# Performance work log

Hardware: AMD Instinct MI355X
Metric: run time of the kernel (lower is better)

Reference implementation:

```python
import jax, jax.numpy as jnp
import numpy as np

# --- static config (matches init_kwargs) ---
CHUNK = 128
MAX_K_QK, MAX_K_V, MAX_K_KNOW = 32, 32, 64
CAND_MULT = 2
N_HEADS = 16


def threshold_gate(scores, tau, max_k):
    """scores:[B,C,N], tau:[B,C,1] -> sparse normalized gates."""
    raw = scores - tau
    gate = jnp.where(raw > 0, raw, 1e-8 * jnp.exp(raw))
    eg = jnp.exp(gate) - 1.0
    topk_vals, _ = jax.lax.top_k(eg, max_k)
    eg = jnp.where(eg >= topk_vals[..., -1:], eg, 0.0)
    gate_sum = eg.sum(axis=-1, keepdims=True) + 1e-8
    gate_strength = jnp.tanh(eg.max(axis=-1, keepdims=True))
    return eg / gate_sum * gate_strength


def _chunked(a, n_chunks):
    B, S = a.shape[0], a.shape[1]
    return a.reshape(B, n_chunks, CHUNK, -1).transpose(1, 0, 2, 3)  # [nc,B,C,*]


def _unchunk(a):
    nc, B, C, D = a.shape
    return a.transpose(1, 0, 2, 3).reshape(B, nc * C, D)


def attn_pipeline(x, qk_pos, v_pos, tau_q, tau_k, tau_v, qk_neurons, v_neurons,
                  npos_qk, npos_v, expand_O):
    B, S, D = x.shape
    n_chunks = S // CHUNK
    n_cq = MAX_K_QK * CAND_MULT
    n_cv = MAX_K_V * CAND_MULT

    xs = (_chunked(x, n_chunks), _chunked(qk_pos, n_chunks), _chunked(v_pos, n_chunks),
          _chunked(tau_q, n_chunks), _chunked(tau_k, n_chunks), _chunked(tau_v, n_chunks))

    def chunk_fn(loss, inp):
        x_c, qp_c, vp_c, tq_c, tk_c, tv_c = inp
        # position-based candidate selection (indices are non-differentiable)
        d_qk = jnp.sum((qp_c[:, :, None, :] - npos_qk[None, None]) ** 2, axis=-1)  # [B,C,Nqk]
        _, idx_qk = jax.lax.top_k(-d_qk, n_cq)
        idx_qk = jax.lax.stop_gradient(idx_qk)
        cand_qk = qk_neurons[idx_qk]                                   # [B,C,n_cq,D]
        d_v = jnp.sum((vp_c[:, :, None, :] - npos_v[None, None]) ** 2, axis=-1)
        _, idx_v = jax.lax.top_k(-d_v, n_cv)
        idx_v = jax.lax.stop_gradient(idx_v)
        cand_v = v_neurons[idx_v]
        # scores == activations here (router dropout is identity, rate 0)
        act_qk = jnp.einsum('bsd,bsnd->bsn', x_c, cand_qk)
        act_v = jnp.einsum('bsd,bsnd->bsn', x_c, cand_v)
        gQ = threshold_gate(act_qk, tq_c, MAX_K_QK)
        gK = threshold_gate(act_qk, tk_c, MAX_K_QK)
        gV = threshold_gate(act_v, tv_c, MAX_K_V)
        Qc = jnp.einsum('bsn,bsnd->bsd', act_qk * gQ, cand_qk)
        Kc = jnp.einsum('bsn,bsnd->bsd', act_qk * gK, cand_qk)
        Vc = jnp.einsum('bsn,bsnd->bsd', act_v * gV, cand_v)
        pl_qk = (jax.lax.stop_gradient(gQ)
                 * jnp.sum((qp_c[:, :, None, :] - npos_qk[idx_qk]) ** 2, axis=-1)).mean()
        pl_v = (jax.lax.stop_gradient(gV)
                * jnp.sum((vp_c[:, :, None, :] - npos_v[idx_v]) ** 2, axis=-1)).mean()
        return loss + pl_qk + pl_v, (Qc, Kc, Vc)

    loss, (Qs, Ks, Vs) = jax.lax.scan(chunk_fn, jnp.float32(0.0), xs)
    Q, K, V = _unchunk(Qs), _unchunk(Ks), _unchunk(Vs)
    pos_loss = loss / n_chunks

    d_head = D // N_HEADS
    Q = Q.reshape(B, S, N_HEADS, d_head).transpose(0, 2, 1, 3)
    K = K.reshape(B, S, N_HEADS, d_head).transpose(0, 2, 1, 3)
    V = V.reshape(B, S, N_HEADS, d_head).transpose(0, 2, 1, 3)
    scores = jnp.einsum('bhsd,bhtd->bhst', Q, K) / jnp.sqrt(jnp.float32(d_head))
    causal = jnp.tril(jnp.ones((S, S), dtype=jnp.bool_))
    scores = jnp.where(causal, scores, jnp.finfo(scores.dtype).min)
    attn_w = jax.nn.softmax(scores, axis=-1)
    out = jnp.einsum('bhst,bhtd->bhsd', attn_w, V)
    out = out.transpose(0, 2, 1, 3).reshape(B, S, D) @ expand_O
    return out, pos_loss


def know_pipeline(x, know_pos, tau, know_neurons, npos_know):
    B, S, D = x.shape
    n_chunks = S // CHUNK
    n_cand = MAX_K_KNOW * CAND_MULT
    xs = (_chunked(x, n_chunks), _chunked(know_pos, n_chunks), _chunked(tau, n_chunks))

    def chunk_fn(loss, inp):
        x_c, p_c, t_c = inp
        dist = jnp.sum((p_c[:, :, None, :] - npos_know[None, None]) ** 2, axis=-1)
        _, idx = jax.lax.top_k(-dist, n_cand)
        idx = jax.lax.stop_gradient(idx)
        cand = know_neurons[idx]                                       # [B,C,n_cand,D]
        act = jnp.einsum('bsd,bsnd->bsn', x_c, cand)
        gate = threshold_gate(act, t_c, MAX_K_KNOW)
        out_c = jnp.einsum('bsn,bsnd->bsd', act * gate, cand)
        pl = (jax.lax.stop_gradient(gate)
              * jnp.sum((p_c[:, :, None, :] - npos_know[idx]) ** 2, axis=-1)).mean()
        return loss + pl, out_c

    loss, outs = jax.lax.scan(chunk_fn, jnp.float32(0.0), xs)
    return _unchunk(outs), loss / n_chunks


def setup_inputs() -> dict:
    key = jax.random.key(0)
    ks = jax.random.split(key, 16)
    B, S, D, P = 1, 1024, 1024, 32
    Nqk, Nv, Nk = 4096, 4096, 8192

    def unit_rows(k, n):
        a = jax.random.normal(k, (n, D), dtype=jnp.float32)
        return a / (jnp.linalg.norm(a, axis=-1, keepdims=True) + 1e-8)

    return {
        'x': jax.random.normal(ks[0], (B, S, D), dtype=jnp.float32),
        'qk_pos': jax.random.normal(ks[1], (B, S, P), dtype=jnp.float32),
        'v_pos': jax.random.normal(ks[2], (B, S, P), dtype=jnp.float32),
        'know_pos': jax.random.normal(ks[3], (B, S, P), dtype=jnp.float32),
        'tau_q': jax.random.uniform(ks[4], (B, S, 1), dtype=jnp.float32),
        'tau_k': jax.random.uniform(ks[5], (B, S, 1), dtype=jnp.float32),
        'tau_v': jax.random.uniform(ks[6], (B, S, 1), dtype=jnp.float32),
        'tau_know': jax.random.uniform(ks[7], (B, S, 1), dtype=jnp.float32),
        'qk_neurons': unit_rows(ks[8], Nqk),
        'v_neurons': unit_rows(ks[9], Nv),
        'know_neurons': unit_rows(ks[10], Nk),
        'npos_qk': jax.random.normal(ks[11], (Nqk, P), dtype=jnp.float32),
        'npos_v': jax.random.normal(ks[12], (Nv, P), dtype=jnp.float32),
        'npos_know': jax.random.normal(ks[13], (Nk, P), dtype=jnp.float32),
        'expand_O': jax.random.normal(ks[14], (D, D), dtype=jnp.float32) * 0.02,
    }


def reference(x, qk_pos, v_pos, know_pos, tau_q, tau_k, tau_v, tau_know,
              qk_neurons, v_neurons, know_neurons, npos_qk, npos_v, npos_know,
              expand_O):
    attn_out, attn_loss = attn_pipeline(x, qk_pos, v_pos, tau_q, tau_k, tau_v,
                                        qk_neurons, v_neurons, npos_qk, npos_v, expand_O)
    h = x + attn_out
    know_out, know_loss = know_pipeline(h, know_pos, tau_know, know_neurons, npos_know)
    out = h + know_out
    return out, attn_loss + know_loss
```

## Files before the change

kernel.cpp:

```cpp
#include <hip/hip_runtime.h>
#include <math.h>

#define S_TOK 1024
#define DMODEL 1024
#define PDIM 32
#define NHEADS 16
#define DHEAD 64

__device__ __forceinline__ float wave_reduce_sum(float v) {
#pragma unroll
  for (int m = 32; m >= 1; m >>= 1) v += __shfl_xor(v, m, 64);
  return v;
}
__device__ __forceinline__ float wave_reduce_max(float v) {
#pragma unroll
  for (int m = 32; m >= 1; m >>= 1) v = fmaxf(v, __shfl_xor(v, m, 64));
  return v;
}
__device__ __forceinline__ float wave_reduce_min(float v) {
#pragma unroll
  for (int m = 32; m >= 1; m >>= 1) v = fminf(v, __shfl_xor(v, m, 64));
  return v;
}

// ... 197 lines not shown
    const int g = tid >> 3, sl = tid & 7;
    const float4 pv = s_p4[sl];
    for (int j = g; j < K; j += 32) {
      const float4 nv =
          *reinterpret_cast<const float4*>(npos + (size_t)s_selidx[j] * PDIM + sl * 4);
      float dx = pv.x - nv.x, dy = pv.y - nv.y, dz = pv.z - nv.z, dw = pv.w - nv.w;
      float d = dx * dx + dy * dy + dz * dz + dw * dw;
      d += __shfl_xor(d, 1, 64);
      d += __shfl_xor(d, 2, 64);
      d += __shfl_xor(d, 4, 64);
      if (sl == 0) s_seldist[j] = d;
    }
  }
  __syncthreads();
  for (int j = tid; j < K; j += 256) {
    out_idx[(size_t)s * K + j] = s_selidx[j];
    out_dist[(size_t)s * K + j] = s_seldist[j];
  }
}

template <int N, int K>
__global__ __launch_bounds__(256) void select_topk_fused_kernel(
    const float* __restrict__ pos, const float* __restrict__ npos,
    int* __restrict__ out_idx, float* __restrict__ out_dist) {
  const int s = blockIdx.x;
  const int tid = threadIdx.x;
  const int lane = tid & 63;
  const int wave = tid >> 6;
  const int sl = lane & 7;
  const int rw = lane >> 3;

  __shared__ float s_dist[N];
  __shared__ unsigned s_hist[NBINS];
  __shared__ unsigned s_part[256];
  __shared__ float4 s_p4[8];
  __shared__ float s_red[16];
  __shared__ float s_lo, s_scale;
  __shared__ int s_B, s_need;
  __shared__ int s_cnt, s_ccnt;
  __shared__ int s_selidx[K];
  __shared__ float s_seldist[K];
  __shared__ int s_cidx[CAND_MAX];
  __shared__ float s_cdist[CAND_MAX];

  if (tid < 8) s_p4[tid] = reinterpret_cast<const float4*>(pos + (size_t)s * PDIM)[tid];
  for (int j = tid; j < K; j += 256) { s_selidx[j] = 0; s_seldist[j] = 0.f; }
  for (int b = tid; b < NBINS; b += 256) s_hist[b] = 0u;
  __syncthreads();

  const float4 pv = s_p4[sl];
  float lmin = 3.0e38f, lmax = -3.0e38f;
  const int rows_per_wave = N / 4;
  const int rbase = wave * rows_per_wave;
  for (int it = 0; it < rows_per_wave; it += 16) {
    const int ra = rbase + it + rw;
    const int rb = ra + 8;
    const float4 na = *reinterpret_cast<const float4*>(npos + (size_t)ra * PDIM + sl * 4);
    const float4 nb = *reinterpret_cast<const float4*>(npos + (size_t)rb * PDIM + sl * 4);
    float dax = pv.x - na.x, day = pv.y - na.y, daz = pv.z - na.z, daw = pv.w - na.w;
    float dbx = pv.x - nb.x, dby = pv.y - nb.y, dbz = pv.z - nb.z, dbw = pv.w - nb.w;
    float da = dax * dax + day * day + daz * daz + daw * daw;
    float db = dbx * dbx + dby * dby + dbz * dbz + dbw * dbw;
    da += __shfl_xor(da, 1, 64); da += __shfl_xor(da, 2, 64); da += __shfl_xor(da, 4, 64);
    db += __shfl_xor(db, 1, 64); db += __shfl_xor(db, 2, 64); db += __shfl_xor(db, 4, 64);
    lmin = fminf(lmin, fminf(da, db));
    lmax = fmaxf(lmax, fmaxf(da, db));
    if (sl == 0) { s_dist[ra] = da; s_dist[rb] = db; }
  }
  lmin = wave_reduce_min(lmin);
  lmax = wave_reduce_max(lmax);
  if (lane == 0) { s_red[wave] = lmin; s_red[8 + wave] = lmax; }
  __syncthreads();
  if (tid == 0) {
    float lo = s_red[0], hi = s_red[8];
    for (int w2 = 1; w2 < 4; ++w2) {
      lo = fminf(lo, s_red[w2]);
      hi = fmaxf(hi, s_red[8 + w2]);
    }
    s_lo = lo;
    s_scale = (float)NBINS / fmaxf(hi - lo, 1e-30f);
  }
  __syncthreads();

  const float lo = s_lo, scale = s_scale;
  for (int n = tid; n < N; n += 256) {
    int b = min(NBINS - 1, (int)((s_dist[n] - lo) * scale));
    atomicAdd(&s_hist[b], 1u);
  }
  __syncthreads();

  unsigned psum = 0;
#pragma unroll 4
  for (int b = tid * 16; b < tid * 16 + 16; ++b) psum += s_hist[b];
  s_part[tid] = psum;
  __syncthreads();
  if (tid == 0) {
    unsigned cum = 0;
    int c = 0;
    for (; c < 256; ++c) {
      unsigned pc = s_part[c];
      if (cum + pc >= (unsigned)K) break;
      cum += pc;
    }
    int b = c * 16;
    for (;; ++b) {
      unsigned cb = s_hist[b];
      if (cum + cb >= (unsigned)K) break;
      cum += cb;
    }
    s_B = b;
    s_need = K - (int)cum;
    s_cnt = 0;
    s_ccnt = 0;
  }
  __syncthreads();

  const int B = s_B;
  for (int n = tid; n < N; n += 256) {
    float d = s_dist[n];
    int b = min(NBINS - 1, (int)((d - lo) * scale));
    if (b < B) {
      int p = atomicAdd(&s_cnt, 1);
      s_selidx[p] = n;
      s_seldist[p] = d;
    } else if (b == B) {
      int e = atomicAdd(&s_ccnt, 1);
      if (e < CAND_MAX) { s_cidx[e] = n; s_cdist[e] = d; }
    }
  }
  __syncthreads();

  const int M = s_ccnt < CAND_MAX ? s_ccnt : CAND_MAX;
  const int need = s_need;
  const int base = s_cnt;
  for (int i = tid; i < M; i += 256) {
    unsigned ki = __float_as_uint(s_cdist[i]);
    int idxi = s_cidx[i];
    int rank = 0;
    for (int j = 0; j < M; ++j) {
      unsigned kj = __float_as_uint(s_cdist[j]);
      rank += (kj < ki || (kj == ki && s_cidx[j] < idxi)) ? 1 : 0;
    }
    if (rank < need) {
      s_selidx[base + rank] = idxi;
      s_seldist[base + rank] = s_cdist[i];
    }
  }
  __syncthreads();

  for (int j = tid; j < K; j += 256) {
    out_idx[(size_t)s * K + j] = s_selidx[j];
    out_dist[(size_t)s * K + j] = s_seldist[j];
  }
}

__global__ __launch_bounds__(256) void attn_token_kernel(
    const float* __restrict__ x,
    const float* __restrict__ tau_q, const float* __restrict__ tau_k,
    const float* __restrict__ tau_v,
    const float* __restrict__ qk_neurons, const float* __restrict__ v_neurons,
    const int* __restrict__ idx_qk, const float* __restrict__ d_qk,
    const int* __restrict__ idx_v, const float* __restrict__ d_v,
    float* __restrict__ Qh, float* __restrict__ Kh, float* __restrict__ Vh,
    float* __restrict__ loss_acc) {
  const int s = blockIdx.x;
  const int tid = threadIdx.x;
  const int lane = tid & 63;
  const int wave = tid >> 6;
  __shared__ __align__(16) float s_x[DMODEL];
  __shared__ float s_act_qk[64], s_act_v[64];
  __shared__ float s_wq[64], s_wk[64], s_wv[64];
  __shared__ float s_gq[64], s_gv[64];
  __shared__ int s_iqk[64], s_iv[64];
  __shared__ int s_qklist[64], s_vlist[64];
  __shared__ int s_qkcnt, s_vcnt;

  for (int i = tid; i < DMODEL; i += 256) s_x[i] = x[(size_t)s * DMODEL + i];
  if (tid < 64) {
    s_iqk[tid] = idx_qk[s * 64 + tid];
    s_iv[tid] = idx_v[s * 64 + tid];
  }
  __syncthreads();

  const float4* x4 = reinterpret_cast<const float4*>(s_x);
  for (int c = wave * 16; c < wave * 16 + 16; ++c) {
    const float4* row4 = reinterpret_cast<const float4*>(qk_neurons + (size_t)s_iqk[c] * DMODEL);
    float acc = 0.f;
#pragma unroll
    for (int k = 0; k < 4; ++k) {
      float4 rv = row4[lane + k * 64];
      float4 xv = x4[lane + k * 64];
      acc += rv.x * xv.x + rv.y * xv.y + rv.z * xv.z + rv.w * xv.w;
    }
    acc = wave_reduce_sum(acc);
    if (lane == 0) s_act_qk[c] = acc;
  }
  for (int c = wave * 16; c < wave * 16 + 16; ++c) {
    const float4* row4 = reinterpret_cast<const float4*>(v_neurons + (size_t)s_iv[c] * DMODEL);
    float acc = 0.f;
#pragma unroll
    for (int k = 0; k < 4; ++k) {
      float4 rv = row4[lane + k * 64];
      float4 xv = x4[lane + k * 64];
      acc += rv.x * xv.x + rv.y * xv.y + rv.z * xv.z + rv.w * xv.w;
    }
    acc = wave_reduce_sum(acc);
    if (lane == 0) s_act_v[c] = acc;
  }
  __syncthreads();

  if (wave < 3) {
    const float a = (wave == 2) ? s_act_v[lane] : s_act_qk[lane];
    const float tau = (wave == 0) ? tau_q[s] : (wave == 1) ? tau_k[s] : tau_v[s];
    float raw = a - tau;
    float gate = (raw > 0.f) ? raw : 1e-8f * __expf(raw);
    float eg = __expf(gate) - 1.f;
    int rank = 0;
    for (int j = 0; j < 64; ++j) {
      float vj = __shfl(eg, j, 64);
      rank += ((vj > eg) || (vj == eg && j < lane)) ? 1 : 0;
    }
    unsigned long long bm = __ballot(rank == 31);
    int srcl = __ffsll(bm) - 1;
    float kthv = __shfl(eg, srcl, 64);
    float w = (eg >= kthv) ? eg : 0.f;
    float gsum = wave_reduce_sum(w) + 1e-8f;
    float strength = tanhf(wave_reduce_max(eg));
    float g = w / gsum * strength;
    if (wave == 0) { s_wq[lane] = a * g; s_gq[lane] = g; }
    else if (wave == 1) { s_wk[lane] = a * g; }
    else { s_wv[lane] = a * g; s_gv[lane] = g; }
  }
  __syncthreads();

  if (wave == 0) {
    bool pred = (s_wq[lane] != 0.f) || (s_wk[lane] != 0.f);
    unsigned long long m = __ballot(pred);
    int pos = __popcll(m & ((1ull << lane) - 1ull));
    if (pred) s_qklist[pos] = lane;
    if (lane == 0) s_qkcnt = __popcll(m);
  } else if (wave == 1) {
    bool pred = (s_wv[lane] != 0.f);
    unsigned long long m = __ballot(pred);
    int pos = __popcll(m & ((1ull << lane) - 1ull));
    if (pred) s_vlist[pos] = lane;
    if (lane == 0) s_vcnt = __popcll(m);
  } else if (wave == 2) {
    float pl = s_gq[lane] * d_qk[s * 64 + lane] + s_gv[lane] * d_v[s * 64 + lane];
    pl = wave_reduce_sum(pl);
    if (lane == 0) atomicAdd(loss_acc, pl * (1.f / 65536.f));
  }
  __syncthreads();

  const int d0 = tid * 4;
  const int nqk = s_qkcnt, nv = s_vcnt;
  float aq0 = 0, aq1 = 0, aq2 = 0, aq3 = 0;
  float ak0 = 0, ak1 = 0, ak2 = 0, ak3 = 0;
  float av0 = 0, av1 = 0, av2 = 0, av3 = 0;
  for (int j = 0; j < nqk; ++j) {
    const int c = s_qklist[j];
    const float4 r = *reinterpret_cast<const float4*>(qk_neurons + (size_t)s_iqk[c] * DMODEL + d0);
    const float wq = s_wq[c], wk = s_wk[c];
    aq0 += wq * r.x; aq1 += wq * r.y; aq2 += wq * r.z; aq3 += wq * r.w;
    ak0 += wk * r.x; ak1 += wk * r.y; ak2 += wk * r.z; ak3 += wk * r.w;
  }
  for (int j = 0; j < nv; ++j) {
    const int c = s_vlist[j];
    const float4 r = *reinterpret_cast<const float4*>(v_neurons + (size_t)s_iv[c] * DMODEL + d0);
    const float wv = s_wv[c];
    av0 += wv * r.x; av1 += wv * r.y; av2 += wv * r.z; av3 += wv * r.w;
  }
  const int hh = d0 >> 6;
  const int dh = d0 & 63;
  const size_t base = ((size_t)hh * S_TOK + s) * DHEAD + dh;
  *reinterpret_cast<float4*>(Qh + base) = make_float4(aq0, aq1, aq2, aq3);
  *reinterpret_cast<float4*>(Kh + base) = make_float4(ak0, ak1, ak2, ak3);
  *reinterpret_cast<float4*>(Vh + base) = make_float4(av0, av1, av2, av3);
}

__global__ __launch_bounds__(256) void attention_partial_kernel(
    const float* __restrict__ Q, const float* __restrict__ K,
    const float* __restrict__ V, float* __restrict__ part) {
  __shared__ float sQ[32][68];
  __shared__ float sKV[64][68];
  __shared__ float sP[32][68];

  const int tid = threadIdx.x;
  const int bid = blockIdx.x;
  const int sw = (bid & 7) * 160 + (bid >> 3);
  const int h = sw / 80;
  const int r80 = sw % 80;
  int qt, c;
  if (r80 < 8) { qt = r80; c = 0; }
  else if (r80 < 24) { qt = 8 + ((r80 - 8) >> 1); c = (r80 - 8) & 1; }
  else if (r80 < 48) { qt = 16 + (r80 - 24) / 3; c = (r80 - 24) % 3; }
  else { qt = 24 + ((r80 - 48) >> 2); c = (r80 - 48) & 3; }
  const int q0 = qt * 32;
  const int kstart = c * 256;
  const int kend = min((qt + 1) * 32, kstart + 256);
  const int ntiles = (kend - kstart + 63) >> 6;
  const int g = qt >> 3;
  const int sbase = qt + 4 * g * (g - 1) + (qt - 8 * g) * g;
  float* slot = part + ((size_t)h * 80 + sbase + c) * 2112;

  const int qp = tid >> 4;
  const int kg = tid & 15;
// ... 261 lines not shown
    float p12 = expf(s12 - mn1), p13 = expf(s13 - mn1);
    float ls0 = p00 + p01 + p02 + p03;
    float ls1 = p10 + p11 + p12 + p13;
#pragma unroll
    for (int mm = 1; mm <= 8; mm <<= 1) {
      ls0 += __shfl_xor(ls0, mm, 64);
      ls1 += __shfl_xor(ls1, mm, 64);
    }
    l0 = l0 * sc0 + ls0;
    l1 = l1 * sc1 + ls1;
    o0.x *= sc0; o0.y *= sc0; o0.z *= sc0; o0.w *= sc0;
    o1.x *= sc1; o1.y *= sc1; o1.z *= sc1; o1.w *= sc1;
    m0 = mn0; m1 = mn1;

    *reinterpret_cast<float4*>(&sP[2 * qp + 0][kg * 4]) = make_float4(p00, p01, p02, p03);
    *reinterpret_cast<float4*>(&sP[2 * qp + 1][kg * 4]) = make_float4(p10, p11, p12, p13);
    __syncthreads();

#pragma unroll
    for (int k4 = 0; k4 < 16; ++k4) {
      float4 pa = *reinterpret_cast<const float4*>(&sP[2 * qp + 0][k4 * 4]);
      float4 pb = *reinterpret_cast<const float4*>(&sP[2 * qp + 1][k4 * 4]);
#pragma unroll
      for (int e = 0; e < 4; ++e) {
        float4 vv = *reinterpret_cast<const float4*>(&sV[k4 * 4 + e][kg * 4]);
        float w0 = (e == 0) ? pa.x : (e == 1) ? pa.y : (e == 2) ? pa.z : pa.w;
        float w1 = (e == 0) ? pb.x : (e == 1) ? pb.y : (e == 2) ? pb.z : pb.w;
        o0.x += w0 * vv.x; o0.y += w0 * vv.y; o0.z += w0 * vv.z; o0.w += w0 * vv.w;
        o1.x += w1 * vv.x; o1.y += w1 * vv.y; o1.z += w1 * vv.z; o1.w += w1 * vv.w;
      }
    }
  }

  const float inv0 = 1.f / l0, inv1 = 1.f / l1;
  float4 r0 = make_float4(o0.x * inv0, o0.y * inv0, o0.z * inv0, o0.w * inv0);
  float4 r1 = make_float4(o1.x * inv1, o1.y * inv1, o1.z * inv1, o1.w * inv1);
  *reinterpret_cast<float4*>(attn_out + (size_t)qg0 * DMODEL + h * DHEAD + kg * 4) = r0;
  *reinterpret_cast<float4*>(attn_out + (size_t)qg1 * DMODEL + h * DHEAD + kg * 4) = r1;
}

__global__ __launch_bounds__(256) void proj_partial_kernel(
    const float* __restrict__ A, const float* __restrict__ Bm,
    float* __restrict__ part) {
  __shared__ float sA[64][68];
  __shared__ float sB[64][68];
  const int tid = threadIdx.x;
  const int tr = tid >> 4, tc = tid & 15;
  const int col0 = blockIdx.x * 64, row0 = blockIdx.y * 64;
  const int z = blockIdx.z;
  const int kbase = z * 256;
  float acc[4][4];
#pragma unroll
  for (int i = 0; i < 4; ++i)
#pragma unroll
    for (int j = 0; j < 4; ++j) acc[i][j] = 0.f;

  for (int kt = 0; kt < 4; ++kt) {
    const int k0 = kbase + kt * 64;
    __syncthreads();
    {
      const float4* Ag = reinterpret_cast<const float4*>(A + (size_t)row0 * DMODEL + k0);
#pragma unroll
      for (int it = 0; it < 4; ++it) {
        int f = tid + it * 256;
        int r = f >> 4, c4 = f & 15;
        *reinterpret_cast<float4*>(&sA[r][c4 * 4]) = Ag[r * 256 + c4];
      }
      const float4* Bg = reinterpret_cast<const float4*>(Bm + (size_t)k0 * DMODEL + col0);
#pragma unroll
      for (int it = 0; it < 4; ++it) {
        int f = tid + it * 256;
        int r = f >> 4, c4 = f & 15;
        *reinterpret_cast<float4*>(&sB[r][c4 * 4]) = Bg[r * 256 + c4];
      }
    }
    __syncthreads();
#pragma unroll 4
    for (int kk = 0; kk < 64; ++kk) {
      float a0 = sA[tr * 4 + 0][kk], a1 = sA[tr * 4 + 1][kk];
      float a2 = sA[tr * 4 + 2][kk], a3 = sA[tr * 4 + 3][kk];
      float4 b = *reinterpret_cast<const float4*>(&sB[kk][tc * 4]);
      acc[0][0] += a0 * b.x; acc[0][1] += a0 * b.y; acc[0][2] += a0 * b.z; acc[0][3] += a0 * b.w;
      acc[1][0] += a1 * b.x; acc[1][1] += a1 * b.y; acc[1][2] += a1 * b.z; acc[1][3] += a1 * b.w;
      acc[2][0] += a2 * b.x; acc[2][1] += a2 * b.y; acc[2][2] += a2 * b.z; acc[2][3] += a2 * b.w;
      acc[3][0] += a3 * b.x; acc[3][1] += a3 * b.y; acc[3][2] += a3 * b.z; acc[3][3] += a3 * b.w;
    }
  }

  float* dst = part + (size_t)z * (DMODEL * S_TOK);
#pragma unroll
  for (int i = 0; i < 4; ++i) {
    *reinterpret_cast<float4*>(dst + (size_t)(row0 + tr * 4 + i) * DMODEL + col0 + tc * 4) =
        make_float4(acc[i][0], acc[i][1], acc[i][2], acc[i][3]);
  }
}

__global__ __launch_bounds__(256) void proj_combine_kernel(
    const float* __restrict__ part, const float* __restrict__ x,
    float* __restrict__ H) {
  const int i = blockIdx.x * 256 + threadIdx.x;
  const float4* p4 = reinterpret_cast<const float4*>(part);
  float4 p0 = p4[i];
  float4 p1 = p4[i + 262144];
  float4 p2 = p4[i + 524288];
  float4 p3 = p4[i + 786432];
  float4 xv = reinterpret_cast<const float4*>(x)[i];
  reinterpret_cast<float4*>(H)[i] =
      make_float4(xv.x + p0.x + p1.x + p2.x + p3.x, xv.y + p0.y + p1.y + p2.y + p3.y,
                  xv.z + p0.z + p1.z + p2.z + p3.z, xv.w + p0.w + p1.w + p2.w + p3.w);
}

__global__ __launch_bounds__(256) void proj_add_kernel(
    const float* __restrict__ A, const float* __restrict__ Bm,
    const float* __restrict__ x, float* __restrict__ H) {
  __shared__ float sA[64][65];
  __shared__ float sB[64][65];
  const int tid = threadIdx.x;
  const int tr = tid >> 4, tc = tid & 15;
  const int row0 = blockIdx.y * 64, col0 = blockIdx.x * 64;
  float acc[4][4];
#pragma unroll
  for (int i = 0; i < 4; ++i)
#pragma unroll
    for (int j = 0; j < 4; ++j) acc[i][j] = 0.f;
  for (int kt = 0; kt < 16; ++kt) {
#pragma unroll
    for (int e = tid; e < 4096; e += 256) {
      int r = e >> 6, c = e & 63;
      sA[r][c] = A[(size_t)(row0 + r) * DMODEL + (kt * 64 + c)];
      sB[r][c] = Bm[(size_t)(kt * 64 + r) * DMODEL + (col0 + c)];
    }
    __syncthreads();
#pragma unroll 4
    for (int kk = 0; kk < 64; ++kk) {
      float a0 = sA[tr * 4 + 0][kk], a1 = sA[tr * 4 + 1][kk];
      float a2 = sA[tr * 4 + 2][kk], a3 = sA[tr * 4 + 3][kk];
      float b0 = sB[kk][tc * 4 + 0], b1 = sB[kk][tc * 4 + 1];
      float b2 = sB[kk][tc * 4 + 2], b3 = sB[kk][tc * 4 + 3];
      acc[0][0] += a0 * b0; acc[0][1] += a0 * b1; acc[0][2] += a0 * b2; acc[0][3] += a0 * b3;
      acc[1][0] += a1 * b0; acc[1][1] += a1 * b1; acc[1][2] += a1 * b2; acc[1][3] += a1 * b3;
      acc[2][0] += a2 * b0; acc[2][1] += a2 * b1; acc[2][2] += a2 * b2; acc[2][3] += a2 * b3;
      acc[3][0] += a3 * b0; acc[3][1] += a3 * b1; acc[3][2] += a3 * b2; acc[3][3] += a3 * b3;
    }
    __syncthreads();
  }
#pragma unroll
  for (int i = 0; i < 4; ++i) {
    size_t ro = (size_t)(row0 + tr * 4 + i) * DMODEL + col0 + tc * 4;
#pragma unroll
    for (int j = 0; j < 4; ++j) H[ro + j] = x[ro + j] + acc[i][j];
  }
}

__global__ __launch_bounds__(256) void know_token_kernel(
    const float* __restrict__ h, const float* __restrict__ tau,
    const float* __restrict__ know_neurons,
    const int* __restrict__ idxk, const float* __restrict__ dk,
    float* __restrict__ out, float* __restrict__ loss_acc) {
  const int s = blockIdx.x;
  const int tid = threadIdx.x;
  const int lane = tid & 63, wave = tid >> 6;
  __shared__ __align__(16) float s_h[DMODEL];
  __shared__ float s_act[128];
  __shared__ float s_eg[128];
  __shared__ float s_w[128];
  __shared__ float s_wg[128];
  __shared__ float s_g[128];
  __shared__ int s_idx[128];
  __shared__ int s_klist[128];
  __shared__ int s_wcnt[2];
  __shared__ int s_kcnt;
  __shared__ float s_kth, s_gsum, s_strength;

  for (int i = tid; i < DMODEL; i += 256) s_h[i] = h[(size_t)s * DMODEL + i];
  if (tid < 128) s_idx[tid] = idxk[s * 128 + tid];
  __syncthreads();

  const float4* h4 = reinterpret_cast<const float4*>(s_h);
  for (int c = wave * 32; c < wave * 32 + 32; ++c) {
    const float4* row4 = reinterpret_cast<const float4*>(know_neurons + (size_t)s_idx[c] * DMODEL);
    float acc = 0.f;
#pragma unroll
    for (int k = 0; k < 4; ++k) {
      float4 rv = row4[lane + k * 64];
      float4 xv = h4[lane + k * 64];
      acc += rv.x * xv.x + rv.y * xv.y + rv.z * xv.z + rv.w * xv.w;
    }
    acc = wave_reduce_sum(acc);
    if (lane == 0) s_act[c] = acc;
  }
  __syncthreads();

  const float tv = tau[s];
  if (tid < 128) {
    float a = s_act[tid];
    float raw = a - tv;
    float gate = (raw > 0.f) ? raw : 1e-8f * __expf(raw);
    s_eg[tid] = __expf(gate) - 1.f;
  }
  __syncthreads();
  if (tid < 128) {
    float e = s_eg[tid];
    int rank = 0;
    for (int j = 0; j < 128; ++j) {
      float ej = s_eg[j];
      rank += ((ej > e) || (ej == e && j < tid)) ? 1 : 0;
    }
    if (rank == 63) s_kth = e;
  }
  __syncthreads();
  if (tid < 128) {
    float e = s_eg[tid];
    s_w[tid] = (e >= s_kth) ? e : 0.f;
  }
  __syncthreads();
  if (wave == 0) {
    float sum = wave_reduce_sum(s_w[lane] + s_w[lane + 64]);
    float mx = wave_reduce_max(fmaxf(s_eg[lane], s_eg[lane + 64]));
    if (lane == 0) { s_gsum = sum + 1e-8f; s_strength = tanhf(mx); }
  }
  if (tid < 128) {
    bool pred = s_w[tid] != 0.f;
    unsigned long long m = __ballot(pred);
    if (lane == 0) s_wcnt[wave] = __popcll(m);
  }
  __syncthreads();
  if (tid < 128) {
    float g = s_w[tid] / s_gsum * s_strength;
    s_g[tid] = g;
    s_wg[tid] = s_act[tid] * g;
    bool pred = s_w[tid] != 0.f;
    unsigned long long m = __ballot(pred);
    int base = (wave == 1) ? s_wcnt[0] : 0;
    int pos = base + __popcll(m & ((1ull << lane) - 1ull));
    if (pred) s_klist[pos] = tid;
    if (tid == 0) s_kcnt = s_wcnt[0] + s_wcnt[1];
  }
  __syncthreads();
  if (wave == 0) {
    float pl = s_g[lane] * dk[s * 128 + lane] + s_g[lane + 64] * dk[s * 128 + lane + 64];
    pl = wave_reduce_sum(pl);
    if (lane == 0) atomicAdd(loss_acc, pl * (1.f / 131072.f));
  }

  const int d0 = tid * 4;
  const int kc = s_kcnt;
  float a0 = 0, a1 = 0, a2 = 0, a3 = 0;
  for (int j = 0; j < kc; ++j) {
    const int c = s_klist[j];
    const float4 r = *reinterpret_cast<const float4*>(know_neurons + (size_t)s_idx[c] * DMODEL + d0);
    const float wv = s_wg[c];
    a0 += wv * r.x; a1 += wv * r.y; a2 += wv * r.z; a3 += wv * r.w;
  }
  float h0 = s_h[d0 + 0], h1 = s_h[d0 + 1], h2 = s_h[d0 + 2], h3 = s_h[d0 + 3];
  *reinterpret_cast<float4*>(out + (size_t)s * DMODEL + d0) =
      make_float4(h0 + a0, h1 + a1, h2 + a2, h3 + a3);
}

extern "C" void kernel_launch(void* const* d_in, const int* in_sizes, int n_in,
                              void* d_out, int out_size, void* d_ws, size_t ws_size,
                              hipStream_t stream) {
  const float* x = (const float*)d_in[0];
  const float* qk_pos = (const float*)d_in[1];
  const float* v_pos = (const float*)d_in[2];
  const float* know_pos = (const float*)d_in[3];
  const float* tau_q = (const float*)d_in[4];
  const float* tau_k = (const float*)d_in[5];
  const float* tau_v = (const float*)d_in[6];
  const float* tau_know = (const float*)d_in[7];
  const float* qk_neurons = (const float*)d_in[8];
  const float* v_neurons = (const float*)d_in[9];
  const float* know_neurons = (const float*)d_in[10];
  const float* npos_qk = (const float*)d_in[11];
  const float* npos_v = (const float*)d_in[12];
  const float* npos_know = (const float*)d_in[13];
  const float* expand_O = (const float*)d_in[14];
  float* out = (float*)d_out;
  float* loss_acc = out + (size_t)S_TOK * DMODEL;

  char* w = (char*)d_ws;
  int* idx_qk = (int*)(w + 0);
  float* dist_qk = (float*)(w + 262144);
  int* idx_v = (int*)(w + 524288);
  float* dist_v = (float*)(w + 786432);
  int* idx_know = (int*)(w + 1048576);
  float* dist_know = (float*)(w + 1572864);
  float* Qb = (float*)(w + 2097152);
  float* Kb = (float*)(w + 6291456);
  float* Vb = (float*)(w + 10485760);
  float* attnbuf = (float*)(w + 14680064);
  float* hbuf = (float*)(w + 18874368);
  float* Rbuf = (float*)(w + 23068672);

  hipMemsetAsync(loss_acc, 0, sizeof(float), stream);

  const bool big_ws = ws_size >= (size_t)23068672 + 16777216;
  if (big_ws) {
    rgemm_kernel<<<dim3(32, 16), 256, 0, stream>>>(qk_pos, npos_qk, Rbuf, 0, 4096);
    select2_kernel<4096, 64><<<1024, 256, 0, stream>>>(Rbuf, qk_pos, npos_qk, 0, idx_qk, dist_qk);
    rgemm_kernel<<<dim3(32, 16), 256, 0, stream>>>(v_pos, npos_v, Rbuf, 0, 4096);
    select2_kernel<4096, 64><<<1024, 256, 0, stream>>>(Rbuf, v_pos, npos_v, 0, idx_v, dist_v);
    rgemm_kernel<<<dim3(64, 8), 256, 0, stream>>>(know_pos, npos_know, Rbuf, 0, 8192);
    select2_kernel<8192, 128><<<512, 256, 0, stream>>>(Rbuf, know_pos, npos_know, 0, idx_know, dist_know);
    rgemm_kernel<<<dim3(64, 8), 256, 0, stream>>>(know_pos, npos_know, Rbuf, 512, 8192);
    select2_kernel<8192, 128><<<512, 256, 0, stream>>>(Rbuf, know_pos, npos_know, 512, idx_know, dist_know);
  } else {
    select_topk_fused_kernel<4096, 64><<<S_TOK, 256, 0, stream>>>(qk_pos, npos_qk, idx_qk, dist_qk);
    select_topk_fused_kernel<4096, 64><<<S_TOK, 256, 0, stream>>>(v_pos, npos_v, idx_v, dist_v);
    select_topk_fused_kernel<8192, 128><<<S_TOK, 256, 0, stream>>>(know_pos, npos_know, idx_know, dist_know);
  }

  attn_token_kernel<<<S_TOK, 256, 0, stream>>>(x, tau_q, tau_k, tau_v, qk_neurons, v_neurons,
                                               idx_qk, dist_qk, idx_v, dist_v, Qb, Kb, Vb, loss_acc);

  if (big_ws) {
    attention_partial_kernel<<<1280, 256, 0, stream>>>(Qb, Kb, Vb, Rbuf);
    attention_combine_kernel<<<512, 256, 0, stream>>>(Rbuf, attnbuf);
    proj_partial_kernel<<<dim3(16, 16, 4), 256, 0, stream>>>(attnbuf, expand_O, Rbuf);
    proj_combine_kernel<<<1024, 256, 0, stream>>>(Rbuf, x, hbuf);
  } else {
    attention_kernel<<<512, 256, 0, stream>>>(Qb, Kb, Vb, attnbuf);
    proj_add_kernel<<<dim3(16, 16), 256, 0, stream>>>(attnbuf, expand_O, x, hbuf);
  }

  know_token_kernel<<<S_TOK, 256, 0, stream>>>(hbuf, tau_know, know_neurons, idx_know, dist_know,
                                               out, loss_acc);
}
```

Measured before the change: 347.2 us.

## Split per-token attn and know kernels into activation and gate/gather stages

In the large-workspace path, the fused per-token attention and knowledge kernels are each split into two kernels. The first computes candidate activations over 2048 blocks (one per token and table or half). The second recomputes the gates and splits the output gather across two blocks per token, each covering half of the model dimension. This exposes more parallelism per token than the previous one-block-per-token kernels. The cost is two extra launches, an activation round trip through global memory, and the gate computation being repeated in both halves.

Measured after the change: 359.1 us. +3.4%, slower.

```diff
diff --git a/kernel.cpp b/kernel.cpp
--- a/kernel.cpp
+++ b/kernel.cpp
@@ -373,6 +373,133 @@
     out_idx[(size_t)s * K + j] = s_selidx[j];
     out_dist[(size_t)s * K + j] = s_seldist[j];
   }
+}
+
+__global__ __launch_bounds__(256) void attn_act_kernel(
+    const float* __restrict__ x,
+    const float* __restrict__ qk_neurons, const float* __restrict__ v_neurons,
+    const int* __restrict__ idx_qk, const int* __restrict__ idx_v,
+    float* __restrict__ actbuf) {
+  const int s = blockIdx.x >> 1;
+  const int tbl = blockIdx.x & 1;
+  const int tid = threadIdx.x, lane = tid & 63, wave = tid >> 6;
+  __shared__ __align__(16) float s_x[DMODEL];
+  __shared__ int s_idx[64];
+  const float* tab = tbl ? v_neurons : qk_neurons;
+  const int* idxp = tbl ? idx_v : idx_qk;
+  for (int i = tid; i < DMODEL; i += 256) s_x[i] = x[(size_t)s * DMODEL + i];
+  if (tid < 64) s_idx[tid] = idxp[s * 64 + tid];
+  __syncthreads();
+  const float4* x4 = reinterpret_cast<const float4*>(s_x);
+  for (int c = wave * 16; c < wave * 16 + 16; ++c) {
+    const float4* row4 = reinterpret_cast<const float4*>(tab + (size_t)s_idx[c] * DMODEL);
+    float acc = 0.f;
+#pragma unroll
+    for (int k = 0; k < 4; ++k) {
+      float4 rv = row4[lane + k * 64];
+      float4 xv = x4[lane + k * 64];
+      acc += rv.x * xv.x + rv.y * xv.y + rv.z * xv.z + rv.w * xv.w;
+    }
+    acc = wave_reduce_sum(acc);
+    if (lane == 0) actbuf[s * 128 + tbl * 64 + c] = acc;
+  }
+}
+
+__global__ __launch_bounds__(256) void attn_gate_kernel(
+    const float* __restrict__ tau_q, const float* __restrict__ tau_k,
+    const float* __restrict__ tau_v,
+    const float* __restrict__ qk_neurons, const float* __restrict__ v_neurons,
+    const int* __restrict__ idx_qk, const float* __restrict__ d_qk,
+    const int* __restrict__ idx_v, const float* __restrict__ d_v,
+    const float* __restrict__ actbuf,
+    float* __restrict__ Qh, float* __restrict__ Kh, float* __restrict__ Vh,
+    float* __restrict__ loss_acc) {
+  const int s = blockIdx.x >> 1;
+  const int dhalf = blockIdx.x & 1;
+  const int tid = threadIdx.x;
+  const int lane = tid & 63;
+  const int wave = tid >> 6;
+  __shared__ float s_act_qk[64], s_act_v[64];
+  __shared__ float s_wq[64], s_wk[64], s_wv[64];
+  __shared__ float s_gq[64], s_gv[64];
+  __shared__ int s_iqk[64], s_iv[64];
+  __shared__ int s_qklist[64], s_vlist[64];
+  __shared__ int s_qkcnt, s_vcnt;
+
+  if (tid < 64) {
+    s_act_qk[tid] = actbuf[s * 128 + tid];
+    s_iqk[tid] = idx_qk[s * 64 + tid];
+  } else if (tid < 128) {
+    s_act_v[tid - 64] = actbuf[s * 128 + tid];
+    s_iv[tid - 64] = idx_v[s * 64 + tid - 64];
+  }
+  __syncthreads();
+
+  if (wave < 3) {
+    const float a = (wave == 2) ? s_act_v[lane] : s_act_qk[lane];
+    const float tau = (wave == 0) ? tau_q[s] : (wave == 1) ? tau_k[s] : tau_v[s];
+    float raw = a - tau;
+    float gate = (raw > 0.f) ? raw : 1e-8f * __expf(raw);
+    float eg = __expf(gate) - 1.f;
+    int rank = 0;
+    for (int j = 0; j < 64; ++j) {
+      float vj = __shfl(eg, j, 64);
+      rank += ((vj > eg) || (vj == eg && j < lane)) ? 1 : 0;
+    }
+    unsigned long long bm = __ballot(rank == 31);
+    int srcl = __ffsll(bm) - 1;
+    float kthv = __shfl(eg, srcl, 64);
+    float w = (eg >= kthv) ? eg : 0.f;
+    float gsum = wave_reduce_sum(w) + 1e-8f;
+    float strength = tanhf(wave_reduce_max(eg));
+    float g = w / gsum * strength;
+    if (wave == 0) { s_wq[lane] = a * g; s_gq[lane] = g; }
+    else if (wave == 1) { s_wk[lane] = a * g; }
+    else { s_wv[lane] = a * g; s_gv[lane] = g; }
+  }
+  __syncthreads();
+
+  if (wave == 0) {
+    bool pred = (s_wq[lane] != 0.f) || (s_wk[lane] != 0.f);
+    unsigned long long m = __ballot(pred);
+    int pos = __popcll(m & ((1ull << lane) - 1ull));
+    if (pred) s_qklist[pos] = lane;
+    if (lane == 0) s_qkcnt = __popcll(m);
+  } else if (wave == 1) {
+    bool pred = (s_wv[lane] != 0.f);
+    unsigned long long m = __ballot(pred);
+    int pos = __popcll(m & ((1ull << lane) - 1ull));
+    if (pred) s_vlist[pos] = lane;
+    if (lane == 0) s_vcnt = __popcll(m);
+  } else if (wave == 2 && dhalf == 0) {
+    float pl = s_gq[lane] * d_qk[s * 64 + lane] + s_gv[lane] * d_v[s * 64 + lane];
+    pl = wave_reduce_sum(pl);
+    if (lane == 0) atomicAdd(loss_acc, pl * (1.f / 65536.f));
+  }
+  __syncthreads();
+
+  const int d0 = dhalf * 512 + tid * 2;
+  const int nqk = s_qkcnt, nv = s_vcnt;
+  float aq0 = 0, aq1 = 0, ak0 = 0, ak1 = 0, av0 = 0, av1 = 0;
+  for (int j = 0; j < nqk; ++j) {
+    const int c = s_qklist[j];
+    const float2 r = *reinterpret_cast<const float2*>(qk_neurons + (size_t)s_iqk[c] * DMODEL + d0);
+    const float wq = s_wq[c], wk = s_wk[c];
+    aq0 += wq * r.x; aq1 += wq * r.y;
+    ak0 += wk * r.x; ak1 += wk * r.y;
+  }
+  for (int j = 0; j < nv; ++j) {
+    const int c = s_vlist[j];
+    const float2 r = *reinterpret_cast<const float2*>(v_neurons + (size_t)s_iv[c] * DMODEL + d0);
+    const float wv = s_wv[c];
+    av0 += wv * r.x; av1 += wv * r.y;
+  }
+  const int hh = d0 >> 6;
+  const int dh = d0 & 63;
+  const size_t base = ((size_t)hh * S_TOK + s) * DHEAD + dh;
+  *reinterpret_cast<float2*>(Qh + base) = make_float2(aq0, aq1);
+  *reinterpret_cast<float2*>(Kh + base) = make_float2(ak0, ak1);
+  *reinterpret_cast<float2*>(Vh + base) = make_float2(av0, av1);
 }
 
 __global__ __launch_bounds__(256) void attn_token_kernel(
@@ -940,6 +1067,124 @@
   }
 }
 
+__global__ __launch_bounds__(256) void know_act_kernel(
+    const float* __restrict__ h, const float* __restrict__ know_neurons,
+    const int* __restrict__ idxk, float* __restrict__ actbuf) {
+  const int s = blockIdx.x >> 1;
+  const int half = blockIdx.x & 1;
+  const int tid = threadIdx.x, lane = tid & 63, wave = tid >> 6;
+  __shared__ __align__(16) float s_h[DMODEL];
+  __shared__ int s_idx[64];
+  for (int i = tid; i < DMODEL; i += 256) s_h[i] = h[(size_t)s * DMODEL + i];
+  if (tid < 64) s_idx[tid] = idxk[s * 128 + half * 64 + tid];
+  __syncthreads();
+  const float4* h4 = reinterpret_cast<const float4*>(s_h);
+  for (int c = wave * 16; c < wave * 16 + 16; ++c) {
+    const float4* row4 = reinterpret_cast<const float4*>(know_neurons + (size_t)s_idx[c] * DMODEL);
+    float acc = 0.f;
+#pragma unroll
+    for (int k = 0; k < 4; ++k) {
+      float4 rv = row4[lane + k * 64];
+      float4 xv = h4[lane + k * 64];
+      acc += rv.x * xv.x + rv.y * xv.y + rv.z * xv.z + rv.w * xv.w;
+    }
+    acc = wave_reduce_sum(acc);
+    if (lane == 0) actbuf[s * 128 + half * 64 + c] = acc;
+  }
+}
+
+__global__ __launch_bounds__(256) void know_gate_kernel(
+    const float* __restrict__ h, const float* __restrict__ tau,
+    const float* __restrict__ know_neurons,
+    const int* __restrict__ idxk, const float* __restrict__ dk,
+    const float* __restrict__ actbuf,
+    float* __restrict__ out, float* __restrict__ loss_acc) {
+  const int s = blockIdx.x >> 1;
+  const int dhalf = blockIdx.x & 1;
+  const int tid = threadIdx.x;
+  const int lane = tid & 63, wave = tid >> 6;
+  __shared__ float s_act[128];
+  __shared__ float s_eg[128];
+  __shared__ float s_w[128];
+  __shared__ float s_wg[128];
+  __shared__ float s_g[128];
+  __shared__ int s_idx[128];
+  __shared__ int s_klist[128];
+  __shared__ int s_wcnt[2];
+  __shared__ int s_kcnt;
+  __shared__ float s_kth, s_gsum, s_strength;
+
+  if (tid < 128) {
+    s_act[tid] = actbuf[s * 128 + tid];
+    s_idx[tid] = idxk[s * 128 + tid];
+  }
+  __syncthreads();
+
+  const float tv = tau[s];
+  if (tid < 128) {
+    float a = s_act[tid];
+    float raw = a - tv;
+    float gate = (raw > 0.f) ? raw : 1e-8f * __expf(raw);
+    s_eg[tid] = __expf(gate) - 1.f;
+  }
+  __syncthreads();
+  if (tid < 128) {
+    float e = s_eg[tid];
+    int rank = 0;
+    for (int j = 0; j < 128; ++j) {
+      float ej = s_eg[j];
+      rank += ((ej > e) || (ej == e && j < tid)) ? 1 : 0;
+    }
+    if (rank == 63) s_kth = e;
+  }
+  __syncthreads();
+  if (tid < 128) {
+    float e = s_eg[tid];
+    s_w[tid] = (e >= s_kth) ? e : 0.f;
+  }
+  __syncthreads();
+  if (wave == 0) {
+    float sum = wave_reduce_sum(s_w[lane] + s_w[lane + 64]);
+    float mx = wave_reduce_max(fmaxf(s_eg[lane], s_eg[lane + 64]));
+    if (lane == 0) { s_gsum = sum + 1e-8f; s_strength = tanhf(mx); }
+  }
+  if (tid < 128) {
+    bool pred = s_w[tid] != 0.f;
+    unsigned long long m = __ballot(pred);
+    if (lane == 0) s_wcnt[wave] = __popcll(m);
+  }
+  __syncthreads();
+  if (tid < 128) {
+    float g = s_w[tid] / s_gsum * s_strength;
+    s_g[tid] = g;
+    s_wg[tid] = s_act[tid] * g;
+    bool pred = s_w[tid] != 0.f;
+    unsigned long long m = __ballot(pred);
+    int base = (wave == 1) ? s_wcnt[0] : 0;
+    int pos = base + __popcll(m & ((1ull << lane) - 1ull));
+    if (pred) s_klist[pos] = tid;
+    if (tid == 0) s_kcnt = s_wcnt[0] + s_wcnt[1];
+  }
+  __syncthreads();
+  if (wave == 0 && dhalf == 0) {
+    float pl = s_g[lane] * dk[s * 128 + lane] + s_g[lane + 64] * dk[s * 128 + lane + 64];
+    pl = wave_reduce_sum(pl);
+    if (lane == 0) atomicAdd(loss_acc, pl * (1.f / 131072.f));
+  }
+
+  const int d0 = dhalf * 512 + tid * 2;
+  const int kc = s_kcnt;
+  float a0 = 0, a1 = 0;
+  for (int j = 0; j < kc; ++j) {
+    const int c = s_klist[j];
+    const float2 r = *reinterpret_cast<const float2*>(know_neurons + (size_t)s_idx[c] * DMODEL + d0);
+    const float wv = s_wg[c];
+    a0 += wv * r.x; a1 += wv * r.y;
+  }
+  const float2 hv = *reinterpret_cast<const float2*>(h + (size_t)s * DMODEL + d0);
+  *reinterpret_cast<float2*>(out + (size_t)s * DMODEL + d0) = make_float2(hv.x + a0, hv.y + a1);
+}
+
 __global__ __launch_bounds__(256) void know_token_kernel(
     const float* __restrict__ h, const float* __restrict__ tau,
     const float* __restrict__ know_neurons,
@@ -1092,25 +1337,30 @@
     select2_kernel<8192, 128><<<512, 256, 0, stream>>>(Rbuf, know_pos, npos_know, 0, idx_know, dist_know);
     rgemm_kernel<<<dim3(64, 8), 256, 0, stream>>>(know_pos, npos_know, Rbuf, 512, 8192);
     select2_kernel<8192, 128><<<512, 256, 0, stream>>>(Rbuf, know_pos, npos_know, 512, idx_know, dist_know);
+
+    attn_act_kernel<<<2048, 256, 0, stream>>>(x, qk_neurons, v_neurons, idx_qk, idx_v, Rbuf);
+    attn_gate_kernel<<<2048, 256, 0, stream>>>(tau_q, tau_k, tau_v, qk_neurons, v_neurons,
+                                               idx_qk, dist_qk, idx_v, dist_v, Rbuf,
+                                               Qb, Kb, Vb, loss_acc);
+
+    attention_partial_kernel<<<1280, 256, 0, stream>>>(Qb, Kb, Vb, Rbuf);
+    attention_combine_kernel<<<512, 256, 0, stream>>>(Rbuf, attnbuf);
+    proj_partial_kernel<<<dim3(16, 16, 4), 256, 0, stream>>>(attnbuf, expand_O, Rbuf);
+    proj_combine_kernel<<<1024, 256, 0, stream>>>(Rbuf, x, hbuf);
+
+    know_act_kernel<<<2048, 256, 0, stream>>>(hbuf, know_neurons, idx_know, Rbuf);
+    know_gate_kernel<<<2048, 256, 0, stream>>>(hbuf, tau_know, know_neurons, idx_know, dist_know,
+                                               Rbuf, out, loss_acc);
   } else {
     select_topk_fused_kernel<4096, 64><<<S_TOK, 256, 0, stream>>>(qk_pos, npos_qk, idx_qk, dist_qk);
     select_topk_fused_kernel<4096, 64><<<S_TOK, 256, 0, stream>>>(v_pos, npos_v, idx_v, dist_v);
     select_topk_fused_kernel<8192, 128><<<S_TOK, 256, 0, stream>>>(know_pos, npos_know, idx_know, dist_know);
-  }
-
-  attn_token_kernel<<<S_TOK, 256, 0, stream>>>(x, tau_q, tau_k, tau_v, qk_neurons, v_neurons,
-                                               idx_qk, dist_qk, idx_v, dist_v, Qb, Kb, Vb, loss_acc);
-
-  if (big_ws) {
-    attention_partial_kernel<<<1280, 256, 0, stream>>>(Qb, Kb, Vb, Rbuf);
-    attention_combine_kernel<<<512, 256, 0, stream>>>(Rbuf, attnbuf);
-    proj_partial_kernel<<<dim3(16, 16, 4), 256, 0, stream>>>(attnbuf, expand_O, Rbuf);
-    proj_combine_kernel<<<1024, 256, 0, stream>>>(Rbuf, x, hbuf);
-  } else {
+
+    attn_token_kernel<<<S_TOK, 256, 0, stream>>>(x, tau_q, tau_k, tau_v, qk_neurons, v_neurons,
+                                                 idx_qk, dist_qk, idx_v, dist_v, Qb, Kb, Vb, loss_acc);
     attention_kernel<<<512, 256, 0, stream>>>(Qb, Kb, Vb, attnbuf);
     proj_add_kernel<<<dim3(16, 16), 256, 0, stream>>>(attnbuf, expand_O, x, hbuf);
-  }
-
-  know_token_kernel<<<S_TOK, 256, 0, stream>>>(hbuf, tau_know, know_neurons, idx_know, dist_know,
-                                               out, loss_acc);
-}
+    know_token_kernel<<<S_TOK, 256, 0, stream>>>(hbuf, tau_know, know_neurons, idx_know, dist_know,
+                                                 out, loss_acc);
+  }
+}
```
